# Kernel optimization log

Hardware: AMD Instinct MI355X
Metric: run time of the kernel (lower is better)

The kernel has to match this reference:

```python
import jax, jax.numpy as jnp
import numpy as np
from jax.scipy.linalg import expm

B, S, D_H, D_C = 8, 1024, 64, 3

def setup_inputs() -> dict:
    key = jax.random.key(0)
    k1, k2, k3 = jax.random.split(key, 3)
    x = jax.random.normal(k1, (B, S, D_H), dtype=jnp.float32)
    r_grid = jax.random.uniform(k2, (B, S, D_C), dtype=jnp.float32)
    L_param = jax.random.normal(k3, (D_C, D_H, D_H), dtype=jnp.float32)
    P_sp = jnp.eye(D_H, dtype=jnp.float32)  # allow_mixing=False -> identity buffer
    return {"x": x, "r_grid": r_grid, "L_param": L_param, "P_sp": P_sp}

def reference(x, r_grid, L_param, P_sp):
    # skew-symmetrize each generator: L_k <- 0.5*(L_k - L_k^T)
    L_skew = 0.5 * (L_param - jnp.swapaxes(L_param, -1, -2))      # [d_c, d_h, d_h]
    # A_r[b,s] = sum_k r_grid[b,s,k] * L_skew[k]
    A_r = jnp.einsum('bsk,kij->bsij', r_grid, L_skew)             # [B, S, d_h, d_h]
    # batched matrix exponential over leading dims
    R_r = expm(A_r)                                               # [B, S, d_h, d_h]
    R_eff = R_r @ P_sp                                            # [B, S, d_h, d_h]
    x_out = jnp.einsum('bsij,bsj->bsi', R_eff, x)                 # [B, S, d_h]
    return x_out
```

## Files before the change

kernel.cpp:

```cpp
#include <hip/hip_runtime.h>


typedef _Float16 half8 __attribute__((ext_vector_type(8)));
typedef __fp16 fp16x2 __attribute__((ext_vector_type(2)));
typedef float float4t __attribute__((ext_vector_type(4)));

union H2U { fp16x2 h; unsigned u; };

__device__ __forceinline__ unsigned pkrtz2(float a, float b) {
    H2U v; v.h = __builtin_amdgcn_cvt_pkrtz(a, b); return v.u;
}
__device__ __forceinline__ float h2lo(unsigned u) { H2U v; v.u = u; return (float)v.h[0]; }
__device__ __forceinline__ float h2hi(unsigned u) { H2U v; v.u = u; return (float)v.h[1]; }


#define PSTR 36

#define STAGE_AND_LOAD_B()                                                       \
  {                                                                              \
    unsigned h0 = pkrtz2(b1[0], b1[1]);                                          \
    unsigned h1 = pkrtz2(b1[2], b1[3]);                                          \
    unsigned l0 = pkrtz2(b1[0] - h2lo(h0), b1[1] - h2hi(h0));                    \
    unsigned l1 = pkrtz2(b1[2] - h2lo(h1), b1[3] - h2hi(h1));                    \
    const int di = 8 * w + 2 * g;                                                \
    *(uint2*)&stage[buf][0][c][di] = make_uint2(h0, h1);                         \
    *(uint2*)&stage[buf][1][c][di] = make_uint2(l0, l1);                         \
    __syncthreads();                                                             \
    _Pragma("unroll")                                                            \
    for (int kt = 0; kt < 2; ++kt) {                                             \
      Bh[kt] = *(const half8*)&stage[buf][0][c][16 * kt + 4 * g];                \
      Bl[kt] = *(const half8*)&stage[buf][1][c][16 * kt + 4 * g];                \
    }                                                                            \
    buf ^= 1;                                                                    \
  }

#define GEMM_COMBINE(TOUT)                                                       \
  {                                                                              \
    _Pragma("unroll")                                                            \
    for (int gen = 0; gen < 3; ++gen) {                                          \
      float q = (gen == 0) ? q0 : ((gen == 1) ? q1 : q2);                        \
      float4t ac0 = {0.f, 0.f, 0.f, 0.f};                                        \
      float4t ac1 = {0.f, 0.f, 0.f, 0.f};                                        \
      ac0 = __builtin_amdgcn_mfma_f32_16x16x32_f16(Ah[gen*2+0], Bh[0], ac0, 0, 0, 0); \
      ac1 = __builtin_amdgcn_mfma_f32_16x16x32_f16(Ah[gen*2+1], Bh[1], ac1, 0, 0, 0); \
      ac0 = __builtin_amdgcn_mfma_f32_16x16x32_f16(Ah[gen*2+0], Bl[0], ac0, 0, 0, 0); \
      ac1 = __builtin_amdgcn_mfma_f32_16x16x32_f16(Ah[gen*2+1], Bl[1], ac1, 0, 0, 0); \
      ac0 = __builtin_amdgcn_mfma_f32_16x16x32_f16(Al[gen*2+0], Bh[0], ac0, 0, 0, 0); \
      ac1 = __builtin_amdgcn_mfma_f32_16x16x32_f16(Al[gen*2+1], Bh[1], ac1, 0, 0, 0); \
      _Pragma("unroll")                                                          \
      for (int r4 = 0; r4 < 4; ++r4) {                                           \
        float sum = ac0[r4] + ac1[r4];                                           \
        if (gen == 0) TOUT[r4] = q * sum;                                        \
        else          TOUT[r4] = fmaf(q, sum, TOUT[r4]);                         \
      }                                                                          \
    }                                                                            \
  }

__global__ __launch_bounds__(256) void liepe_mfma(
    const float* __restrict__ x,
    const float* __restrict__ r_grid,
    const float* __restrict__ L_param,
    float* __restrict__ out,
    int n_tokens)
{
    __shared__ __align__(16) unsigned stage[2][2][16][PSTR];

    const int lane = threadIdx.x & 63;
    const int w    = threadIdx.x >> 6;
    const int c    = lane & 15;
    const int g    = lane >> 4;

    int tok = blockIdx.x * 16 + c;
    if (tok >= n_tokens) tok = n_tokens - 1;

    half8 Ah[6], Al[6];
    {
        const int i = 16 * w + (lane & 15);
        #pragma unroll
        for (int gen = 0; gen < 3; ++gen) {
            const float* Lg = L_param + gen * 4096;
            #pragma unroll
            for (int kt = 0; kt < 2; ++kt) {
                const int kk0 = 32 * kt + 8 * g;
                half8 hi, lo;
                #pragma unroll
                for (int j = 0; j < 8; ++j) {
                    int kk = kk0 + j;
                    float d = Lg[i * 64 + kk] - Lg[kk * 64 + i];
                    _Float16 h = (_Float16)d;
                    hi[j] = h;
                    lo[j] = (_Float16)(d - (float)h);
                }
                Ah[gen * 2 + kt] = hi;
                Al[gen * 2 + kt] = lo;
            }
        }
    }

    float xv[4];
    {
        float4 v = *(const float4*)(x + tok * 64 + 16 * w + 4 * g);
        xv[0] = v.x; xv[1] = v.y; xv[2] = v.z; xv[3] = v.w;
    }

    const float r0 = r_grid[tok * 3 + 0];
    const float r1 = r_grid[tok * 3 + 1];
    const float r2 = r_grid[tok * 3 + 2];
    const float sig2 = 0.5f * (r0 * r0 + r1 * r1 + r2 * r2);
    const float rho  = fmaf(17.3f, __builtin_sqrtf(sig2), 2.0f);
    const float inv_rho = 1.0f / rho;
    const int   M  = (int)rho + 12;
    const int   ms = M + 10;
    const float q0 = r0 * inv_rho, q1 = r1 * inv_rho, q2 = r2 * inv_rho;

    int maxM = M;
    #pragma unroll
    for (int off = 1; off < 64; off <<= 1)
        maxM = max(maxM, __shfl_xor(maxM, off));

    float jp = 0.f, jc = 0.f, N = 0.f;
    float b1[4] = {0.f, 0.f, 0.f, 0.f};
    float b2[4] = {0.f, 0.f, 0.f, 0.f};

    #pragma unroll 1
    for (int m = maxM + 10; m > maxM; --m) {
        bool sd = (m == ms);
        jc = sd ? 1e-12f : jc;
        jp = sd ? 0.f : jp;
        N  = sd ? (((m & 1) == 0) ? 2e-12f : 0.f) : N;
        float s = (jc > 1.0f) ? __builtin_amdgcn_rcpf(jc) : 1.0f;
        jc *= s; jp *= s; N *= s;
        float jm = fmaf((2.f * (float)m) * inv_rho, jc, -jp);
        jp = jc; jc = jm;
        int mm = m - 1;
        if ((mm & 1) == 0) N += (mm > 0) ? (jm + jm) : jm;
    }

    half8 Bh[2], Bl[2];
    int buf = 0;

    #pragma unroll 1
    for (int m = maxM; m >= 1; --m) {
        bool sd = (m == ms);
        jc = sd ? 1e-12f : jc;
        jp = sd ? 0.f : jp;
        N  = sd ? (((m & 1) == 0) ? 2e-12f : 0.f) : N;

        float s = (jc > 1.0f) ? __builtin_amdgcn_rcpf(jc) : 1.0f;
        jc *= s; jp *= s; N *= s;
        #pragma unroll
        for (int i = 0; i < 4; ++i) { b1[i] *= s; b2[i] *= s; }

        STAGE_AND_LOAD_B();

        float t[4];
        GEMM_COMBINE(t);

        float cf = (m <= M) ? (jc + jc) : 0.f;
        #pragma unroll
        for (int i = 0; i < 4; ++i) {
            float bn = fmaf(cf, xv[i], t[i] + b2[i]);
            b2[i] = b1[i];
            b1[i] = bn;
        }

        float jm = fmaf((2.f * (float)m) * inv_rho, jc, -jp);
        jp = jc; jc = jm;
        int mm = m - 1;
        if ((mm & 1) == 0) N += (mm > 0) ? (jm + jm) : jm;
    }

    {
        STAGE_AND_LOAD_B();
        float t[4];
        GEMM_COMBINE(t);
        float4 v;
        float y0 = fmaf(jc, xv[0], t[0] + b2[0]);
        float y1 = fmaf(jc, xv[1], t[1] + b2[1]);
        float y2 = fmaf(jc, xv[2], t[2] + b2[2]);
        float y3 = fmaf(jc, xv[3], t[3] + b2[3]);
        v.x = (y0 - 0.5f * t[0]) / N;
        v.y = (y1 - 0.5f * t[1]) / N;
        v.z = (y2 - 0.5f * t[2]) / N;
        v.w = (y3 - 0.5f * t[3]) / N;
        *(float4*)(out + tok * 64 + 16 * w + 4 * g) = v;
    }
}

extern "C" void kernel_launch(void* const* d_in, const int* in_sizes, int n_in,
                              void* d_out, int out_size, void* d_ws, size_t ws_size,
                              hipStream_t stream) {
    const float* x = (const float*)d_in[0];
    const float* r = (const float*)d_in[1];
    const float* L = (const float*)d_in[2];
    float* out = (float*)d_out;

    int n_tokens = in_sizes[0] / 64;

    int nwg = (n_tokens + 15) / 16;
    liepe_mfma<<<nwg, 256, 0, stream>>>(x, r, L, out, n_tokens);
}
```

Baseline: 29.77 us.

## Use 2 waves per block, each computing two 16-row output tiles

Halves the block from 4 waves to 2, so each wave now owns two 16-row slices of the 64x64 generator product. It holds twice as many A fragments and accumulators in registers and issues twice as many MFMAs per iteration. The aim is to cut barrier cost and per-block duplicated scalar recurrence work, and to raise MFMA issue density per wave. In exchange it roughly doubles VGPR use (waves_per_eu limited to 1-2) and lowers the number of waves per CU that can hide latency.

```diff
diff --git a/kernel.cpp b/kernel.cpp
--- a/kernel.cpp
+++ b/kernel.cpp
@@ -18,13 +18,16 @@
 
 #define STAGE_AND_LOAD_B()                                                       \
   {                                                                              \
-    unsigned h0 = pkrtz2(b1[0], b1[1]);                                          \
-    unsigned h1 = pkrtz2(b1[2], b1[3]);                                          \
-    unsigned l0 = pkrtz2(b1[0] - h2lo(h0), b1[1] - h2hi(h0));                    \
-    unsigned l1 = pkrtz2(b1[2] - h2lo(h1), b1[3] - h2hi(h1));                    \
-    const int di = 8 * w + 2 * g;                                                \
-    *(uint2*)&stage[buf][0][c][di] = make_uint2(h0, h1);                         \
-    *(uint2*)&stage[buf][1][c][di] = make_uint2(l0, l1);                         \
+    _Pragma("unroll")                                                            \
+    for (int t2 = 0; t2 < 2; ++t2) {                                             \
+      unsigned h0 = pkrtz2(b1[4*t2+0], b1[4*t2+1]);                              \
+      unsigned h1 = pkrtz2(b1[4*t2+2], b1[4*t2+3]);                              \
+      unsigned l0 = pkrtz2(b1[4*t2+0] - h2lo(h0), b1[4*t2+1] - h2hi(h0));        \
+      unsigned l1 = pkrtz2(b1[4*t2+2] - h2lo(h1), b1[4*t2+3] - h2hi(h1));        \
+      const int di = 8 * (2 * w + t2) + 2 * g;                                   \
+      *(uint2*)&stage[buf][0][c][di] = make_uint2(h0, h1);                       \
+      *(uint2*)&stage[buf][1][c][di] = make_uint2(l0, l1);                       \
+    }                                                                            \
     __syncthreads();                                                             \
     _Pragma("unroll")                                                            \
     for (int kt = 0; kt < 2; ++kt) {                                             \
@@ -37,26 +40,32 @@
 #define GEMM_COMBINE(TOUT)                                                       \
   {                                                                              \
     _Pragma("unroll")                                                            \
-    for (int gen = 0; gen < 3; ++gen) {                                          \
-      float q = (gen == 0) ? q0 : ((gen == 1) ? q1 : q2);                        \
-      float4t ac0 = {0.f, 0.f, 0.f, 0.f};                                        \
-      float4t ac1 = {0.f, 0.f, 0.f, 0.f};                                        \
-      ac0 = __builtin_amdgcn_mfma_f32_16x16x32_f16(Ah[gen*2+0], Bh[0], ac0, 0, 0, 0); \
-      ac1 = __builtin_amdgcn_mfma_f32_16x16x32_f16(Ah[gen*2+1], Bh[1], ac1, 0, 0, 0); \
-      ac0 = __builtin_amdgcn_mfma_f32_16x16x32_f16(Ah[gen*2+0], Bl[0], ac0, 0, 0, 0); \
-      ac1 = __builtin_amdgcn_mfma_f32_16x16x32_f16(Ah[gen*2+1], Bl[1], ac1, 0, 0, 0); \
-      ac0 = __builtin_amdgcn_mfma_f32_16x16x32_f16(Al[gen*2+0], Bh[0], ac0, 0, 0, 0); \
-      ac1 = __builtin_amdgcn_mfma_f32_16x16x32_f16(Al[gen*2+1], Bh[1], ac1, 0, 0, 0); \
+    for (int t2 = 0; t2 < 2; ++t2) {                                             \
       _Pragma("unroll")                                                          \
-      for (int r4 = 0; r4 < 4; ++r4) {                                           \
-        float sum = ac0[r4] + ac1[r4];                                           \
-        if (gen == 0) TOUT[r4] = q * sum;                                        \
-        else          TOUT[r4] = fmaf(q, sum, TOUT[r4]);                         \
+      for (int gen = 0; gen < 3; ++gen) {                                        \
+        float q = (gen == 0) ? q0 : ((gen == 1) ? q1 : q2);                      \
+        const int f0 = gen * 4 + t2 * 2;                                         \
+        float4t ac0 = {0.f, 0.f, 0.f, 0.f};                                      \
+        float4t ac1 = {0.f, 0.f, 0.f, 0.f};                                      \
+        ac0 = __builtin_amdgcn_mfma_f32_16x16x32_f16(Ah[f0+0], Bh[0], ac0, 0, 0, 0); \
+        ac1 = __builtin_amdgcn_mfma_f32_16x16x32_f16(Ah[f0+1], Bh[1], ac1, 0, 0, 0); \
+        ac0 = __builtin_amdgcn_mfma_f32_16x16x32_f16(Ah[f0+0], Bl[0], ac0, 0, 0, 0); \
+        ac1 = __builtin_amdgcn_mfma_f32_16x16x32_f16(Ah[f0+1], Bl[1], ac1, 0, 0, 0); \
+        ac0 = __builtin_amdgcn_mfma_f32_16x16x32_f16(Al[f0+0], Bh[0], ac0, 0, 0, 0); \
+        ac1 = __builtin_amdgcn_mfma_f32_16x16x32_f16(Al[f0+1], Bh[1], ac1, 0, 0, 0); \
+        _Pragma("unroll")                                                        \
+        for (int r4 = 0; r4 < 4; ++r4) {                                         \
+          float sum = ac0[r4] + ac1[r4];                                         \
+          if (gen == 0) TOUT[t2 * 4 + r4] = q * sum;                             \
+          else          TOUT[t2 * 4 + r4] = fmaf(q, sum, TOUT[t2 * 4 + r4]);     \
+        }                                                                        \
       }                                                                          \
     }                                                                            \
   }
 
-__global__ __launch_bounds__(256) void liepe_mfma(
+__global__ __launch_bounds__(128)
+__attribute__((amdgpu_waves_per_eu(1, 2)))
+void liepe_mfma(
     const float* __restrict__ x,
     const float* __restrict__ r_grid,
     const float* __restrict__ L_param,
@@ -73,34 +82,39 @@
     int tok = blockIdx.x * 16 + c;
     if (tok >= n_tokens) tok = n_tokens - 1;
 
-    half8 Ah[6], Al[6];
+    half8 Ah[12], Al[12];
     {
-        const int i = 16 * w + (lane & 15);
-        #pragma unroll
-        for (int gen = 0; gen < 3; ++gen) {
-            const float* Lg = L_param + gen * 4096;
+        #pragma unroll
+        for (int t2 = 0; t2 < 2; ++t2) {
+            const int i = 16 * (2 * w + t2) + (lane & 15);
             #pragma unroll
-            for (int kt = 0; kt < 2; ++kt) {
-                const int kk0 = 32 * kt + 8 * g;
-                half8 hi, lo;
+            for (int gen = 0; gen < 3; ++gen) {
+                const float* Lg = L_param + gen * 4096;
                 #pragma unroll
-                for (int j = 0; j < 8; ++j) {
-                    int kk = kk0 + j;
-                    float d = Lg[i * 64 + kk] - Lg[kk * 64 + i];
-                    _Float16 h = (_Float16)d;
-                    hi[j] = h;
-                    lo[j] = (_Float16)(d - (float)h);
+                for (int kt = 0; kt < 2; ++kt) {
+                    const int kk0 = 32 * kt + 8 * g;
+                    half8 hi, lo;
+                    #pragma unroll
+                    for (int j = 0; j < 8; ++j) {
+                        int kk = kk0 + j;
+                        float d = Lg[i * 64 + kk] - Lg[kk * 64 + i];
+                        _Float16 h = (_Float16)d;
+                        hi[j] = h;
+                        lo[j] = (_Float16)(d - (float)h);
+                    }
+                    Ah[gen * 4 + t2 * 2 + kt] = hi;
+                    Al[gen * 4 + t2 * 2 + kt] = lo;
                 }
-                Ah[gen * 2 + kt] = hi;
-                Al[gen * 2 + kt] = lo;
             }
         }
     }
 
-    float xv[4];
-    {
-        float4 v = *(const float4*)(x + tok * 64 + 16 * w + 4 * g);
-        xv[0] = v.x; xv[1] = v.y; xv[2] = v.z; xv[3] = v.w;
+    float xv[8];
+    #pragma unroll
+    for (int t2 = 0; t2 < 2; ++t2) {
+        float4 v = *(const float4*)(x + tok * 64 + 16 * (2 * w + t2) + 4 * g);
+        xv[4 * t2 + 0] = v.x; xv[4 * t2 + 1] = v.y;
+        xv[4 * t2 + 2] = v.z; xv[4 * t2 + 3] = v.w;
     }
 
     const float r0 = r_grid[tok * 3 + 0];
@@ -119,8 +133,8 @@
         maxM = max(maxM, __shfl_xor(maxM, off));
 
     float jp = 0.f, jc = 0.f, N = 0.f;
-    float b1[4] = {0.f, 0.f, 0.f, 0.f};
-    float b2[4] = {0.f, 0.f, 0.f, 0.f};
+    float b1[8] = {0.f, 0.f, 0.f, 0.f, 0.f, 0.f, 0.f, 0.f};
+    float b2[8] = {0.f, 0.f, 0.f, 0.f, 0.f, 0.f, 0.f, 0.f};
 
     #pragma unroll 1
     for (int m = maxM + 10; m > maxM; --m) {
@@ -149,16 +163,16 @@
         float s = (jc > 1.0f) ? __builtin_amdgcn_rcpf(jc) : 1.0f;
         jc *= s; jp *= s; N *= s;
         #pragma unroll
-        for (int i = 0; i < 4; ++i) { b1[i] *= s; b2[i] *= s; }
+        for (int i = 0; i < 8; ++i) { b1[i] *= s; b2[i] *= s; }
 
         STAGE_AND_LOAD_B();
 
-        float t[4];
+        float t[8];
         GEMM_COMBINE(t);
 
         float cf = (m <= M) ? (jc + jc) : 0.f;
         #pragma unroll
-        for (int i = 0; i < 4; ++i) {
+        for (int i = 0; i < 8; ++i) {
             float bn = fmaf(cf, xv[i], t[i] + b2[i]);
             b2[i] = b1[i];
             b1[i] = bn;
@@ -172,18 +186,21 @@
 
     {
         STAGE_AND_LOAD_B();
-        float t[4];
+        float t[8];
         GEMM_COMBINE(t);
-        float4 v;
-        float y0 = fmaf(jc, xv[0], t[0] + b2[0]);
-        float y1 = fmaf(jc, xv[1], t[1] + b2[1]);
-        float y2 = fmaf(jc, xv[2], t[2] + b2[2]);
-        float y3 = fmaf(jc, xv[3], t[3] + b2[3]);
-        v.x = (y0 - 0.5f * t[0]) / N;
-        v.y = (y1 - 0.5f * t[1]) / N;
-        v.z = (y2 - 0.5f * t[2]) / N;
-        v.w = (y3 - 0.5f * t[3]) / N;
-        *(float4*)(out + tok * 64 + 16 * w + 4 * g) = v;
+        #pragma unroll
+        for (int t2 = 0; t2 < 2; ++t2) {
+            float4 v;
+            float y0 = fmaf(jc, xv[4*t2+0], t[4*t2+0] + b2[4*t2+0]);
+            float y1 = fmaf(jc, xv[4*t2+1], t[4*t2+1] + b2[4*t2+1]);
+            float y2 = fmaf(jc, xv[4*t2+2], t[4*t2+2] + b2[4*t2+2]);
+            float y3 = fmaf(jc, xv[4*t2+3], t[4*t2+3] + b2[4*t2+3]);
+            v.x = (y0 - 0.5f * t[4*t2+0]) / N;
+            v.y = (y1 - 0.5f * t[4*t2+1]) / N;
+            v.z = (y2 - 0.5f * t[4*t2+2]) / N;
+            v.w = (y3 - 0.5f * t[4*t2+3]) / N;
+            *(float4*)(out + tok * 64 + 16 * (2 * w + t2) + 4 * g) = v;
+        }
     }
 }
 
@@ -198,5 +215,5 @@
     int n_tokens = in_sizes[0] / 64;
 
     int nwg = (n_tokens + 15) / 16;
-    liepe_mfma<<<nwg, 256, 0, stream>>>(x, r, L, out, n_tokens);
+    liepe_mfma<<<nwg, 128, 0, stream>>>(x, r, L, out, n_tokens);
 }
```

Measured after the change: 36.13 us. 21.4% more time.
